# Performance work log

Hardware: AMD Instinct MI355X
Metric: run time of the kernel (lower is better)

The kernel has to match this reference:

```python
import jax, jax.numpy as jnp
import numpy as np

B, L, DM = 1, 512, 768
DS, DC, EX = 64, 4, 2
DI = EX * DM            # d_inner = 1536
DR = DM // 16           # dt_rank = 48


def setup_inputs() -> dict:
    key = jax.random.key(0)
    ks = jax.random.split(key, 12)
    s = 0.02
    inp = {
        "x": jax.random.normal(ks[0], (B, L, DM), dtype=jnp.float32),
        "ln_w": jnp.ones((DM,), jnp.float32),
        "ln_b": jnp.zeros((DM,), jnp.float32),
        "in_proj_w": jax.random.normal(ks[1], (2 * DI, DM), jnp.float32) * s,
        "conv_w": jax.random.normal(ks[2], (DI, 1, DC), jnp.float32) * s,
        "conv_b": jnp.zeros((DI,), jnp.float32),
        "x_proj_w": jax.random.normal(ks[3], (DR + 2 * DS, DI), jnp.float32) * s,
        "dt_proj_w": jax.random.normal(ks[4], (DI, DR), jnp.float32) * s,
        "dt_proj_b": jax.random.normal(ks[5], (DI,), jnp.float32) * s,
        "A_log": jnp.log(jnp.broadcast_to(jnp.arange(1, DS + 1, dtype=jnp.float32), (DI, DS))),
        "D": jnp.ones((DI,), jnp.float32),
        "out_proj_w": jax.random.normal(ks[6], (DM, DI), jnp.float32) * s,
    }
    return inp


def _layernorm(x, w, b, eps=1e-5):
    mu = jnp.mean(x, axis=-1, keepdims=True)
    var = jnp.mean((x - mu) ** 2, axis=-1, keepdims=True)
    return (x - mu) * jax.lax.rsqrt(var + eps) * w + b


def _causal_depthwise_conv(x, w, b):
    # x: [B, L, DI] -> conv over time, depthwise, causal (left pad DC-1)
    xc = jnp.transpose(x, (0, 2, 1))  # [B, DI, L]
    y = jax.lax.conv_general_dilated(
        xc, w, window_strides=(1,), padding=[(DC - 1, 0)],
        dimension_numbers=("NCH", "OIH", "NCH"), feature_group_count=DI)
    y = y + b[None, :, None]
    return jnp.transpose(y, (0, 2, 1))  # [B, L, DI]


def _selective_scan(deltaA, deltaB_u, C):
    # deltaA, deltaB_u: [B, L, DI, DS]; C: [B, L, DS]
    dA = jnp.transpose(deltaA, (1, 0, 2, 3))
    dBu = jnp.transpose(deltaB_u, (1, 0, 2, 3))
    Ct = jnp.transpose(C, (1, 0, 2))
    s0 = jnp.zeros(deltaA.shape[:1] + deltaA.shape[2:], deltaA.dtype).transpose(0, 1, 2)
    s0 = jnp.zeros((deltaA.shape[0], deltaA.shape[2], deltaA.shape[3]), deltaA.dtype)

    def step(s, inp):
        dA_t, dBu_t, C_t = inp
        s = dA_t * s + dBu_t                      # [B, DI, DS]
        y = jnp.einsum("bdn,bn->bd", s, C_t)      # [B, DI]
        return s, y

    _, ys = jax.lax.scan(step, s0, (dA, dBu, Ct))
    return jnp.transpose(ys, (1, 0, 2))           # [B, L, DI]


def reference(x, ln_w, ln_b, in_proj_w, conv_w, conv_b, x_proj_w,
              dt_proj_w, dt_proj_b, A_log, D, out_proj_w):
    residual = x
    h = _layernorm(x, ln_w, ln_b)
    xz = jnp.einsum("bld,ed->ble", h, in_proj_w)  # [B, L, 2*DI]
    x_in, z = jnp.split(xz, 2, axis=-1)
    x_in = jax.nn.silu(_causal_depthwise_conv(x_in, conv_w, conv_b))
    x_dbl = jnp.einsum("bld,ed->ble", x_in, x_proj_w)  # [B, L, DR+2*DS]
    dt, Bm, Cm = jnp.split(x_dbl, [DR, DR + DS], axis=-1)
    dt = jax.nn.softplus(jnp.einsum("blr,dr->bld", dt, dt_proj_w) + dt_proj_b)  # [B,L,DI]
    A = -jnp.exp(A_log)                                 # [DI, DS]
    deltaA = jnp.exp(dt[..., None] * A)                 # [B, L, DI, DS]
    deltaB_u = dt[..., None] * Bm[:, :, None, :] * x_in[..., None]
    y = _selective_scan(deltaA, deltaB_u, Cm)           # [B, L, DI]
    y = y + x_in * D
    y = y * jax.nn.silu(z)
    out = jnp.einsum("bld,ed->ble", y, out_proj_w)      # [B, L, DM]
    return residual + out
```

## Files before the change

kernel.cpp:

```cpp
#include <hip/hip_runtime.h>
#include <hip/hip_bf16.h>
#include <math.h>

#define L_SEQ 512
#define DM 768
#define DI 1536
#define DS 64
#define DC 4
#define DR 48
#define NBC 128
#define NP2 (NBC + DI)
#define NC 8
#define TC 64

typedef __attribute__((ext_vector_type(8))) short short8;
typedef __attribute__((ext_vector_type(4))) float float4v;

#define J_LN 512
#define J_WI (2 * DI * DM / 1024)
#define J_WBC (NBC * DI / 1024)
#define J_WO (DM * DI / 1024)
#define J_WEFF ((DI / 64) * (DI / 64))
#define PREP_GRID (J_LN + J_WI + J_WBC + J_WO + J_WEFF)

__device__ __forceinline__ float bp_add(float p, int addr) {
  return p + __int_as_float(__builtin_amdgcn_ds_bpermute(addr, __float_as_int(p)));
}
__device__ __forceinline__ float lane_read(float v, int t) {
  return __int_as_float(__builtin_amdgcn_readlane(__float_as_int(v), t));
}
__device__ __forceinline__ short f2bf(float v) {
  __hip_bfloat16 h = __float2bfloat16(v);
  return *reinterpret_cast<short*>(&h);
}
__device__ __forceinline__ short8 cvt8f(const float* p, bool valid) {
  float4 u = *(const float4*)(p);
  float4 v = *(const float4*)(p + 4);
  short8 r;
  r[0] = f2bf(u.x); r[1] = f2bf(u.y); r[2] = f2bf(u.z); r[3] = f2bf(u.w);
  r[4] = f2bf(v.x); r[5] = f2bf(v.y); r[6] = f2bf(v.z); r[7] = f2bf(v.w);
  if (!valid) r = (short8)0;
  return r;
}
__device__ __forceinline__ void cvt_blk(const float* __restrict__ s,
                                        short* __restrict__ d, int b) {
  int i = b * 1024 + threadIdx.x * 4;
  float4 v = *(const float4*)(s + i);
  short4 o; o.x = f2bf(v.x); o.y = f2bf(v.y); o.z = f2bf(v.z); o.w = f2bf(v.w);
  *(short4*)(d + i) = o;
}

__device__ __forceinline__ float4v gemm32_core(
    const short* __restrict__ A, int lda, const short* __restrict__ B, int ldb,
    int K, int bx, int by, int lane, int w, float4v* red) {
  int ks = K >> 2;
  int kbeg = w * ks;
  int fr = lane & 15, koff = (lane >> 4) * 8;
  int m0 = by * 32, n0 = bx * 32;
  const short* pA0 = A + (size_t)(m0 + fr) * lda + koff + kbeg;
  const short* pA1 = pA0 + (size_t)16 * lda;
  const short* pB0 = B + (size_t)(n0 + fr) * ldb + koff + kbeg;
  const short* pB1 = pB0 + (size_t)16 * ldb;
  float4v acc00 = (float4v){0.f,0.f,0.f,0.f}, acc01 = acc00;
  float4v acc10 = acc00, acc11 = acc00;
  short8 a0A = *(const short8*)(pA0);      short8 a1A = *(const short8*)(pA1);
  short8 b0A = *(const short8*)(pB0);      short8 b1A = *(const short8*)(pB1);
  short8 a0B = *(const short8*)(pA0 + 32); short8 a1B = *(const short8*)(pA1 + 32);
  short8 b0B = *(const short8*)(pB0 + 32); short8 b1B = *(const short8*)(pB1 + 32);
  for (int k0 = 0; k0 < ks; k0 += 64) {
    short8 ca0 = a0A, ca1 = a1A, cb0 = b0A, cb1 = b1A;
    short8 da0 = a0B, da1 = a1B, db0 = b0B, db1 = b1B;
    int nA = k0 + 64; if (nA >= ks) nA = 0;
    int nB = k0 + 96; if (nB >= ks) nB = 32;
    a0A = *(const short8*)(pA0 + nA); a1A = *(const short8*)(pA1 + nA);
    b0A = *(const short8*)(pB0 + nA); b1A = *(const short8*)(pB1 + nA);
    a0B = *(const short8*)(pA0 + nB); a1B = *(const short8*)(pA1 + nB);
    b0B = *(const short8*)(pB0 + nB); b1B = *(const short8*)(pB1 + nB);
    acc00 = __builtin_amdgcn_mfma_f32_16x16x32_bf16(ca0, cb0, acc00, 0, 0, 0);
    acc01 = __builtin_amdgcn_mfma_f32_16x16x32_bf16(ca0, cb1, acc01, 0, 0, 0);
    acc10 = __builtin_amdgcn_mfma_f32_16x16x32_bf16(ca1, cb0, acc10, 0, 0, 0);
    acc11 = __builtin_amdgcn_mfma_f32_16x16x32_bf16(ca1, cb1, acc11, 0, 0, 0);
    acc00 = __builtin_amdgcn_mfma_f32_16x16x32_bf16(da0, db0, acc00, 0, 0, 0);
    acc01 = __builtin_amdgcn_mfma_f32_16x16x32_bf16(da0, db1, acc01, 0, 0, 0);
    acc10 = __builtin_amdgcn_mfma_f32_16x16x32_bf16(da1, db0, acc10, 0, 0, 0);
    acc11 = __builtin_amdgcn_mfma_f32_16x16x32_bf16(da1, db1, acc11, 0, 0, 0);
  }
  red[(w * 4 + 0) * 64 + lane] = acc00;
  red[(w * 4 + 1) * 64 + lane] = acc01;
  red[(w * 4 + 2) * 64 + lane] = acc10;
  red[(w * 4 + 3) * 64 + lane] = acc11;
  __syncthreads();
  float4v v = red[(0 * 4 + w) * 64 + lane];
  v = v + red[(1 * 4 + w) * 64 + lane];
  v = v + red[(2 * 4 + w) * 64 + lane];
  v = v + red[(3 * 4 + w) * 64 + lane];
  return v;
}

__device__ __forceinline__ void trans_store32(float* t, float4v v,
                                              int lrow, int lcol, int tid,
                                              float* dst, size_t ldT, int m0) {
  __syncthreads();
#pragma unroll
  for (int r = 0; r < 4; ++r) t[lcol * 33 + lrow + r] = v[r];
  __syncthreads();
  int i = tid >> 3, j = (tid & 7) * 4;
  float4 o = make_float4(t[i * 33 + j], t[i * 33 + j + 1],
                         t[i * 33 + j + 2], t[i * 33 + j + 3]);
  *(float4*)&dst[(size_t)i * ldT + m0 + j] = o;
}

__global__ __launch_bounds__(256) void prep(
    const float* __restrict__ x, const float* __restrict__ lnw,
    const float* __restrict__ lnb, short* __restrict__ h,
    const float* __restrict__ wi, short* __restrict__ wib,
    const float* __restrict__ wx, const float* __restrict__ wdt,
    short* __restrict__ wcomb, const float* __restrict__ wo,
    short* __restrict__ wob) {
  __shared__ float ls[4], ls2[4];
  int b = blockIdx.x;
  int tid = threadIdx.x, lane = tid & 63, w = tid >> 6;
  if (b < J_LN) {
    int l = b;
    const float* xr = x + l * DM;
    float s = 0.f, s2 = 0.f;
    for (int i = tid; i < DM; i += 256) { float t = xr[i]; s += t; s2 += t * t; }
#pragma unroll
    for (int off = 32; off; off >>= 1) { s += __shfl_xor(s, off); s2 += __shfl_xor(s2, off); }
    if (lane == 0) { ls[w] = s; ls2[w] = s2; }
    __syncthreads();
    s = ls[0] + ls[1] + ls[2] + ls[3];
    s2 = ls2[0] + ls2[1] + ls2[2] + ls2[3];
    float mean = s * (1.f / DM);
    float var = s2 * (1.f / DM) - mean * mean;
    float rstd = rsqrtf(var + 1e-5f);
    for (int i = tid; i < DM; i += 256)
      h[l * DM + i] = f2bf((xr[i] - mean) * rstd * lnw[i] + lnb[i]);
    return;
  }
  b -= J_LN;
  if (b < J_WI) { cvt_blk(wi, wib, b); return; }
  b -= J_WI;
  if (b < J_WBC) { cvt_blk(wx + DR * DI, wcomb, b); return; }
  b -= J_WBC;
  if (b < J_WO) { cvt_blk(wo, wob, b); return; }
  b -= J_WO;
  {
    int tm = b / (DI / 64), tn = b % (DI / 64);
    int qi = w & 1, qj = w >> 1;
    int m0 = tm * 64 + qi * 32, n0 = tn * 64 + qj * 32;
    int fr = lane & 15, koff = (lane >> 4) * 8;
    const float* pA0 = wdt + (size_t)(m0 + fr) * DR;
    const float* pA1 = pA0 + (size_t)16 * DR;
    float4v a00 = (float4v){0.f,0.f,0.f,0.f}, a01 = a00, a10 = a00, a11 = a00;
#pragma unroll
    for (int k0 = 0; k0 < 64; k0 += 32) {
      bool valid = (k0 + koff) < DR;
      int off = valid ? k0 + koff : 0;
      short8 fa0 = cvt8f(pA0 + off, valid);
      short8 fa1 = cvt8f(pA1 + off, valid);
      short8 fb0, fb1;
#pragma unroll
      for (int j = 0; j < 8; ++j) {
        int r = k0 + koff + j;
        fb0[j] = valid ? f2bf(wx[(size_t)r * DI + n0 + fr]) : (short)0;
        fb1[j] = valid ? f2bf(wx[(size_t)r * DI + n0 + 16 + fr]) : (short)0;
      }
      a00 = __builtin_amdgcn_mfma_f32_16x16x32_bf16(fa0, fb0, a00, 0, 0, 0);
      a01 = __builtin_amdgcn_mfma_f32_16x16x32_bf16(fa0, fb1, a01, 0, 0, 0);
      a10 = __builtin_amdgcn_mfma_f32_16x16x32_bf16(fa1, fb0, a10, 0, 0, 0);
      a11 = __builtin_amdgcn_mfma_f32_16x16x32_bf16(fa1, fb1, a11, 0, 0, 0);
    }
    int rb = (lane >> 4) * 4, cb = lane & 15;
#pragma unroll
    for (int r = 0; r < 4; ++r) {
      wcomb[(size_t)(NBC + m0 + rb + r) * DI + n0 + cb]      = f2bf(a00[r]);
      wcomb[(size_t)(NBC + m0 + rb + r) * DI + n0 + 16 + cb] = f2bf(a01[r]);
      wcomb[(size_t)(NBC + m0 + 16 + rb + r) * DI + n0 + cb]      = f2bf(a10[r]);
      wcomb[(size_t)(NBC + m0 + 16 + rb + r) * DI + n0 + 16 + cb] = f2bf(a11[r]);
    }
  }
}

__global__ __launch_bounds__(256) void k_inproj(const short* __restrict__ h,
                                                const short* __restrict__ wi,
                                                float* __restrict__ xz_in,
                                                float* __restrict__ zt) {
  __shared__ float4v red[16 * 64];
  int tid = threadIdx.x, lane = tid & 63, w = tid >> 6;
  float4v v = gemm32_core(h, DM, wi, DM, DM, blockIdx.x, blockIdx.y, lane, w, red);
  int lrow = ((w & 1) << 4) + ((lane >> 4) << 2);
  int lcol = ((w >> 1) << 4) + (lane & 15);
  int m0 = blockIdx.y * 32, n0 = blockIdx.x * 32;
  if (n0 < DI) {
#pragma unroll
    for (int r = 0; r < 4; ++r)
      xz_in[(size_t)(m0 + lrow + r) * DI + n0 + lcol] = v[r];
  } else {
    trans_store32((float*)red, v, lrow, lcol, tid,
                  zt + (size_t)(n0 - DI) * L_SEQ, L_SEQ, m0);
  }
}

__global__ __launch_bounds__(256) void conv_silu_kernel(const float* __restrict__ xz_in,
                                                        const float* __restrict__ cw,
                                                        const float* __restrict__ cb,
                                                        short* __restrict__ xc_bf,
                                                        float* __restrict__ xct) {
  __shared__ float t2[64 * 34];
  int tid = threadIdx.x;
  int dloc = tid & 63, lseg = tid >> 6;
  int d0 = blockIdx.x * 64, l0 = blockIdx.y * 32;
  int d = d0 + dloc;
  int lb = l0 + lseg * 8;
  float xin[11];
#pragma unroll
  for (int i = 0; i < 11; ++i) {
    int l = lb - 3 + i;
    xin[i] = (l >= 0) ? xz_in[(size_t)l * DI + d] : 0.f;
  }
  float w0 = cw[d * 4 + 0], w1 = cw[d * 4 + 1];
  float w2 = cw[d * 4 + 2], w3 = cw[d * 4 + 3];
  float bias = cb[d];
#pragma unroll
  for (int j = 0; j < 8; ++j) {
    float acc = bias;
    acc = fmaf(w0, xin[j], acc);
    acc = fmaf(w1, xin[j + 1], acc);
    acc = fmaf(w2, xin[j + 2], acc);
    acc = fmaf(w3, xin[j + 3], acc);
    float sig = 1.f / (1.f + __expf(-acc));
    float v = acc * sig;
    xc_bf[(size_t)(lb + j) * DI + d] = f2bf(v);
    t2[dloc * 34 + lseg * 8 + j] = v;
  }
  __syncthreads();
  int row = tid >> 2, j4 = (tid & 3) * 8;
  const float* src = &t2[row * 34 + j4];
  float2 o0 = *(const float2*)(src + 0);
  float2 o1 = *(const float2*)(src + 2);
  float2 o2 = *(const float2*)(src + 4);
  float2 o3 = *(const float2*)(src + 6);
  float* dst = &xct[(size_t)(d0 + row) * L_SEQ + l0 + j4];
  *(float2*)(dst + 0) = o0; *(float2*)(dst + 2) = o1;
  *(float2*)(dst + 4) = o2; *(float2*)(dst + 6) = o3;
}

__global__ __launch_bounds__(256) void k_proj2(const short* __restrict__ xc,
                                               const short* __restrict__ wcomb,
                                               float* __restrict__ xdblBC,
                                               float* __restrict__ dtt,
                                               const float* __restrict__ bias) {
  __shared__ float4v red[16 * 64];
  int tid = threadIdx.x, lane = tid & 63, w = tid >> 6;
  float4v v = gemm32_core(xc, DI, wcomb, DI, DI, blockIdx.x, blockIdx.y,
                          lane, w, red);
  int lrow = ((w & 1) << 4) + ((lane >> 4) << 2);
  int lcol = ((w >> 1) << 4) + (lane & 15);
  int m0 = blockIdx.y * 32, n0 = blockIdx.x * 32;
  if (n0 < NBC) {
#pragma unroll
    for (int r = 0; r < 4; ++r)
      xdblBC[(size_t)(m0 + lrow + r) * NBC + n0 + lcol] = v[r];
  } else {
    float bi = bias[n0 - NBC + lcol];
#pragma unroll
    for (int r = 0; r < 4; ++r) {
      float t = v[r] + bi;
      v[r] = (t > 20.f) ? t : log1pf(__expf(t));
    }
    trans_store32((float*)red, v, lrow, lcol, tid,
                  dtt + (size_t)(n0 - NBC) * L_SEQ, L_SEQ, m0);
  }
}

__global__ __launch_bounds__(256) void scan_p1(const float* __restrict__ dtt,
                                               const float* __restrict__ xct,
                                               const float* __restrict__ xdblBC,
                                               const float* __restrict__ A_log,
                                               float* __restrict__ send,
                                               float* __restrict__ dts) {
  int lane = threadIdx.x & 63;
  int wid = threadIdx.x >> 6;
  int pair = blockIdx.x * 4 + wid;
  int c = __builtin_amdgcn_readfirstlane(pair / DI);
  int d = __builtin_amdgcn_readfirstlane(pair - (pair / DI) * DI);
  float A = -__expf(A_log[(size_t)d * DS + lane]);
  int l0 = c * TC;
  float dtv = dtt[(size_t)d * L_SEQ + l0 + lane];
  float xv  = xct[(size_t)d * L_SEQ + l0 + lane];
  const float* pB = xdblBC + (size_t)l0 * NBC + lane;
  float s = 0.f;
#pragma unroll 8
  for (int t = 0; t < TC; ++t) {
    float dt_c = lane_read(dtv, t);
    float x_c  = lane_read(xv, t);
    float B_c  = pB[(size_t)t * NBC];
    float dA = __expf(dt_c * A);
    s = fmaf(dA, s, dt_c * x_c * B_c);
  }
  float dsum = dtv;
  dsum = bp_add(dsum, (lane ^ 1) << 2);  dsum = bp_add(dsum, (lane ^ 2) << 2);
  dsum = bp_add(dsum, (lane ^ 4) << 2);  dsum = bp_add(dsum, (lane ^ 8) << 2);
  dsum = bp_add(dsum, (lane ^ 16) << 2); dsum = bp_add(dsum, (lane ^ 32) << 2);
  send[((size_t)c * DI + d) * DS + lane] = s;
  if (lane == 0) dts[c * DI + d] = dsum;
}

__global__ __launch_bounds__(256) void scan_p3(const float* __restrict__ dtt,
                                               const float* __restrict__ xct,
                                               const float* __restrict__ xdblBC,
                                               const float* __restrict__ A_log,
                                               const float* __restrict__ Dv,
                                               const float* __restrict__ zt,
                                               const float* __restrict__ send,
                                               const float* __restrict__ dts,
                                               short* __restrict__ y) {
  __shared__ float Pb[4][16][66];
  __shared__ float ys[64][5];
  int tid = threadIdx.x;
  int lane = tid & 63;
  int wid = tid >> 6;
  int pair = blockIdx.x * 4 + wid;
  int c = __builtin_amdgcn_readfirstlane(pair / DI);
  int d = __builtin_amdgcn_readfirstlane(pair - (pair / DI) * DI);
  float A = -__expf(A_log[(size_t)d * DS + lane]);
  float Dd = Dv[d];
  int l0 = c * TC;
  float dtv = dtt[(size_t)d * L_SEQ + l0 + lane];
  float xv  = xct[(size_t)d * L_SEQ + l0 + lane];
  float zv  = zt[(size_t)d * L_SEQ + l0 + lane];
  float s = 0.f;
  for (int cc = 0; cc < c; ++cc) {
    float P = __expf(A * dts[cc * DI + d]);
    s = fmaf(P, s, send[((size_t)cc * DI + d) * DS + lane]);
  }
  const float* pB = xdblBC + (size_t)l0 * NBC + lane;
  float yv = 0.f;
#pragma unroll
  for (int sb = 0; sb < 4; ++sb) {
    float P[16];
#pragma unroll
    for (int j = 0; j < 16; ++j) {
      int t = sb * 16 + j;
      float dt_c = lane_read(dtv, t);
      float x_c  = lane_read(xv, t);
      float B_c  = pB[(size_t)t * NBC];
      float C_c  = pB[(size_t)t * NBC + DS];
      float dA = __expf(dt_c * A);
      s = fmaf(dA, s, dt_c * x_c * B_c);
      P[j] = s * C_c;
    }
#pragma unroll
    for (int j = 0; j < 16; ++j) Pb[wid][j][lane] = P[j];
    int t4 = lane >> 2, q = lane & 3;
    const float* row = &Pb[wid][t4][q * 16];
    float part = 0.f;
#pragma unroll
    for (int k = 0; k < 8; ++k) {
      float2 v2 = *(const float2*)(row + 2 * k);
      part += v2.x + v2.y;
    }
    part = bp_add(part, (lane ^ 1) << 2);
    part = bp_add(part, (lane ^ 2) << 2);
    float got = __int_as_float(
        __builtin_amdgcn_ds_bpermute((lane & 15) << 4, __float_as_int(part)));
    yv = ((lane >> 4) == sb) ? got : yv;
  }
  float sig = 1.f / (1.f + __expf(-zv));
  ys[lane][wid] = (yv + xv * Dd) * (zv * sig);
  __syncthreads();
  if (tid < 64) {
    int d0 = (blockIdx.x * 4) % DI;
    short4 o;
    o.x = f2bf(ys[tid][0]); o.y = f2bf(ys[tid][1]);
    o.z = f2bf(ys[tid][2]); o.w = f2bf(ys[tid][3]);
    *(short4*)&y[(size_t)(l0 + tid) * DI + d0] = o;
  }
}

__global__ __launch_bounds__(256) void k_outproj(const short* __restrict__ y,
                                                 const short* __restrict__ wo,
                                                 const float* __restrict__ x,
                                                 float* __restrict__ out) {
  __shared__ float4v red[16 * 64];
  int tid = threadIdx.x, lane = tid & 63, w = tid >> 6;
  float4v v = gemm32_core(y, DI, wo, DI, DI, blockIdx.x, blockIdx.y, lane, w, red);
  int lrow = ((w & 1) << 4) + ((lane >> 4) << 2);
  int lcol = ((w >> 1) << 4) + (lane & 15);
  int row = blockIdx.y * 32 + lrow, col = blockIdx.x * 32 + lcol;
#pragma unroll
  for (int r = 0; r < 4; ++r)
    out[(size_t)(row + r) * DM + col] = v[r] + x[(size_t)(row + r) * DM + col];
}

extern "C" void kernel_launch(void* const* d_in, const int* in_sizes, int n_in,
                              void* d_out, int out_size, void* d_ws, size_t ws_size,
                              hipStream_t stream) {
  const float* x         = (const float*)d_in[0];
  const float* ln_w      = (const float*)d_in[1];
  const float* ln_b      = (const float*)d_in[2];
  const float* in_proj_w = (const float*)d_in[3];
  const float* conv_w    = (const float*)d_in[4];
  const float* conv_b    = (const float*)d_in[5];
  const float* x_proj_w  = (const float*)d_in[6];
  const float* dt_proj_w = (const float*)d_in[7];
  const float* dt_proj_b = (const float*)d_in[8];
  const float* A_log     = (const float*)d_in[9];
  const float* Dv        = (const float*)d_in[10];
  const float* out_proj_w= (const float*)d_in[11];
  float* out = (float*)d_out;

  float* ws = (float*)d_ws;
  float* xz_in  = ws;
  float* zt     = xz_in + 786432;
  float* xct    = zt + 786432;
  float* dtt    = xct + 786432;
  float* xdblBC = dtt + 786432;
  float* send   = xdblBC + 65536;
  float* dts    = send + 688128;
  float* fend   = dts + 10752;
  short* h_bf   = (short*)fend;
  short* wi_bf  = h_bf + 393216;
  short* wo_bf  = wi_bf + 2359296;
  short* wcomb  = wo_bf + 1179648;
  short* xc_bf  = wcomb + 2555904;
  short* y_bf   = xc_bf + 786432;

  prep<<<PREP_GRID, 256, 0, stream>>>(x, ln_w, ln_b, h_bf, in_proj_w, wi_bf,
                                      x_proj_w, dt_proj_w, wcomb,
                                      out_proj_w, wo_bf);

  k_inproj<<<dim3(2 * DI / 32, L_SEQ / 32), 256, 0, stream>>>(h_bf, wi_bf,
                                                              xz_in, zt);

  conv_silu_kernel<<<dim3(DI / 64, L_SEQ / 32), 256, 0, stream>>>(
      xz_in, conv_w, conv_b, xc_bf, xct);

  k_proj2<<<dim3(NP2 / 32, L_SEQ / 32), 256, 0, stream>>>(
      xc_bf, wcomb, xdblBC, dtt, dt_proj_b);

  scan_p1<<<((NC - 1) * DI) / 4, 256, 0, stream>>>(dtt, xct, xdblBC, A_log,
                                                   send, dts);
  scan_p3<<<(NC * DI) / 4, 256, 0, stream>>>(dtt, xct, xdblBC, A_log, Dv, zt,
                                             send, dts, y_bf);

  k_outproj<<<dim3(DM / 32, L_SEQ / 32), 256, 0, stream>>>(y_bf, wo_bf, x, out);
}
```

Before: 187.6 us.

## Fuse two-pass chunked scan into one block-level kernel with shared-memory carry

```diff
diff --git a/kernel.cpp b/kernel.cpp
--- a/kernel.cpp
+++ b/kernel.cpp
@@ -10,8 +10,8 @@
 #define DR 48
 #define NBC 128
 #define NP2 (NBC + DI)
-#define NC 8
-#define TC 64
+#define NCF 4
+#define TCF 128
 
 typedef __attribute__((ext_vector_type(8))) short short8;
 typedef __attribute__((ext_vector_type(4))) float float4v;
@@ -274,109 +274,113 @@
   }
 }
 
-__global__ __launch_bounds__(256) void scan_p1(const float* __restrict__ dtt,
-                                               const float* __restrict__ xct,
-                                               const float* __restrict__ xdblBC,
-                                               const float* __restrict__ A_log,
-                                               float* __restrict__ send,
-                                               float* __restrict__ dts) {
-  int lane = threadIdx.x & 63;
-  int wid = threadIdx.x >> 6;
-  int pair = blockIdx.x * 4 + wid;
-  int c = __builtin_amdgcn_readfirstlane(pair / DI);
-  int d = __builtin_amdgcn_readfirstlane(pair - (pair / DI) * DI);
-  float A = -__expf(A_log[(size_t)d * DS + lane]);
-  int l0 = c * TC;
-  float dtv = dtt[(size_t)d * L_SEQ + l0 + lane];
-  float xv  = xct[(size_t)d * L_SEQ + l0 + lane];
-  const float* pB = xdblBC + (size_t)l0 * NBC + lane;
-  float s = 0.f;
-#pragma unroll 8
-  for (int t = 0; t < TC; ++t) {
-    float dt_c = lane_read(dtv, t);
-    float x_c  = lane_read(xv, t);
-    float B_c  = pB[(size_t)t * NBC];
-    float dA = __expf(dt_c * A);
-    s = fmaf(dA, s, dt_c * x_c * B_c);
-  }
-  float dsum = dtv;
-  dsum = bp_add(dsum, (lane ^ 1) << 2);  dsum = bp_add(dsum, (lane ^ 2) << 2);
-  dsum = bp_add(dsum, (lane ^ 4) << 2);  dsum = bp_add(dsum, (lane ^ 8) << 2);
-  dsum = bp_add(dsum, (lane ^ 16) << 2); dsum = bp_add(dsum, (lane ^ 32) << 2);
-  send[((size_t)c * DI + d) * DS + lane] = s;
-  if (lane == 0) dts[c * DI + d] = dsum;
-}
-
-__global__ __launch_bounds__(256) void scan_p3(const float* __restrict__ dtt,
-                                               const float* __restrict__ xct,
-                                               const float* __restrict__ xdblBC,
-                                               const float* __restrict__ A_log,
-                                               const float* __restrict__ Dv,
-                                               const float* __restrict__ zt,
-                                               const float* __restrict__ send,
-                                               const float* __restrict__ dts,
-                                               short* __restrict__ y) {
-  __shared__ float Pb[4][16][66];
-  __shared__ float ys[64][5];
+__global__ __launch_bounds__(512) void scan_fused(const float* __restrict__ dtt,
+                                                  const float* __restrict__ xct,
+                                                  const float* __restrict__ xdblBC,
+                                                  const float* __restrict__ A_log,
+                                                  const float* __restrict__ Dv,
+                                                  const float* __restrict__ zt,
+                                                  short* __restrict__ y) {
+  __shared__ float Pb[8][16][66];
+  __shared__ float sendL[2][4][64];
+  __shared__ float dtsL[2][4];
+  __shared__ float ys[2][512];
   int tid = threadIdx.x;
   int lane = tid & 63;
-  int wid = tid >> 6;
-  int pair = blockIdx.x * 4 + wid;
-  int c = __builtin_amdgcn_readfirstlane(pair / DI);
-  int d = __builtin_amdgcn_readfirstlane(pair - (pair / DI) * DI);
+  int wv = tid >> 6;
+  int dloc = wv >> 2;
+  int c = wv & 3;
+  int d = blockIdx.x * 2 + dloc;
   float A = -__expf(A_log[(size_t)d * DS + lane]);
-  float Dd = Dv[d];
-  int l0 = c * TC;
-  float dtv = dtt[(size_t)d * L_SEQ + l0 + lane];
-  float xv  = xct[(size_t)d * L_SEQ + l0 + lane];
-  float zv  = zt[(size_t)d * L_SEQ + l0 + lane];
+  int l0 = c * TCF;
+  const float* dtp = dtt + (size_t)d * L_SEQ + l0;
+  const float* xp  = xct + (size_t)d * L_SEQ + l0;
+  const float* zp  = zt  + (size_t)d * L_SEQ + l0;
+  float dtv0 = dtp[lane], dtv1 = dtp[64 + lane];
+  float xv0  = xp[lane],  xv1  = xp[64 + lane];
+  float zv0  = zp[lane],  zv1  = zp[64 + lane];
+  const float* pB = xdblBC + (size_t)l0 * NBC + lane;
+
+  if (c < 3) {
+    float s = 0.f;
+#pragma unroll 8
+    for (int t = 0; t < 64; ++t) {
+      float dt_c = lane_read(dtv0, t);
+      float x_c  = lane_read(xv0, t);
+      float B_c  = pB[(size_t)t * NBC];
+      s = fmaf(__expf(dt_c * A), s, dt_c * x_c * B_c);
+    }
+#pragma unroll 8
+    for (int t = 0; t < 64; ++t) {
+      float dt_c = lane_read(dtv1, t);
+      float x_c  = lane_read(xv1, t);
+      float B_c  = pB[(size_t)(64 + t) * NBC];
+      s = fmaf(__expf(dt_c * A), s, dt_c * x_c * B_c);
+    }
+    float dsum = dtv0 + dtv1;
+    dsum = bp_add(dsum, (lane ^ 1) << 2);  dsum = bp_add(dsum, (lane ^ 2) << 2);
+    dsum = bp_add(dsum, (lane ^ 4) << 2);  dsum = bp_add(dsum, (lane ^ 8) << 2);
+    dsum = bp_add(dsum, (lane ^ 16) << 2); dsum = bp_add(dsum, (lane ^ 32) << 2);
+    sendL[dloc][c][lane] = s;
+    if (lane == 0) dtsL[dloc][c] = dsum;
+  }
+  __syncthreads();
+
   float s = 0.f;
   for (int cc = 0; cc < c; ++cc) {
-    float P = __expf(A * dts[cc * DI + d]);
-    s = fmaf(P, s, send[((size_t)cc * DI + d) * DS + lane]);
-  }
-  const float* pB = xdblBC + (size_t)l0 * NBC + lane;
-  float yv = 0.f;
-#pragma unroll
-  for (int sb = 0; sb < 4; ++sb) {
-    float P[16];
-#pragma unroll
-    for (int j = 0; j < 16; ++j) {
-      int t = sb * 16 + j;
-      float dt_c = lane_read(dtv, t);
-      float x_c  = lane_read(xv, t);
-      float B_c  = pB[(size_t)t * NBC];
-      float C_c  = pB[(size_t)t * NBC + DS];
-      float dA = __expf(dt_c * A);
-      s = fmaf(dA, s, dt_c * x_c * B_c);
-      P[j] = s * C_c;
-    }
-#pragma unroll
-    for (int j = 0; j < 16; ++j) Pb[wid][j][lane] = P[j];
-    int t4 = lane >> 2, q = lane & 3;
-    const float* row = &Pb[wid][t4][q * 16];
-    float part = 0.f;
-#pragma unroll
-    for (int k = 0; k < 8; ++k) {
-      float2 v2 = *(const float2*)(row + 2 * k);
-      part += v2.x + v2.y;
-    }
-    part = bp_add(part, (lane ^ 1) << 2);
-    part = bp_add(part, (lane ^ 2) << 2);
-    float got = __int_as_float(
-        __builtin_amdgcn_ds_bpermute((lane & 15) << 4, __float_as_int(part)));
-    yv = ((lane >> 4) == sb) ? got : yv;
-  }
-  float sig = 1.f / (1.f + __expf(-zv));
-  ys[lane][wid] = (yv + xv * Dd) * (zv * sig);
-  __syncthreads();
-  if (tid < 64) {
-    int d0 = (blockIdx.x * 4) % DI;
-    short4 o;
-    o.x = f2bf(ys[tid][0]); o.y = f2bf(ys[tid][1]);
-    o.z = f2bf(ys[tid][2]); o.w = f2bf(ys[tid][3]);
-    *(short4*)&y[(size_t)(l0 + tid) * DI + d0] = o;
-  }
+    float P = __expf(A * dtsL[dloc][cc]);
+    s = fmaf(P, s, sendL[dloc][cc][lane]);
+  }
+
+  float yout0 = 0.f, yout1 = 0.f;
+#pragma unroll
+  for (int half = 0; half < 2; ++half) {
+    float dtvh = half ? dtv1 : dtv0;
+    float xvh  = half ? xv1 : xv0;
+    float yv = 0.f;
+#pragma unroll
+    for (int sb = 0; sb < 4; ++sb) {
+      float P[16];
+#pragma unroll
+      for (int j = 0; j < 16; ++j) {
+        int t = sb * 16 + j;
+        float dt_c = lane_read(dtvh, t);
+        float x_c  = lane_read(xvh, t);
+        float B_c  = pB[(size_t)(half * 64 + t) * NBC];
+        float C_c  = pB[(size_t)(half * 64 + t) * NBC + DS];
+        s = fmaf(__expf(dt_c * A), s, dt_c * x_c * B_c);
+        P[j] = s * C_c;
+      }
+#pragma unroll
+      for (int j = 0; j < 16; ++j) Pb[wv][j][lane] = P[j];
+      int t4 = lane >> 2, q = lane & 3;
+      const float* row = &Pb[wv][t4][q * 16];
+      float part = 0.f;
+#pragma unroll
+      for (int k = 0; k < 8; ++k) {
+        float2 v2 = *(const float2*)(row + 2 * k);
+        part += v2.x + v2.y;
+      }
+      part = bp_add(part, (lane ^ 1) << 2);
+      part = bp_add(part, (lane ^ 2) << 2);
+      float got = __int_as_float(
+          __builtin_amdgcn_ds_bpermute((lane & 15) << 4, __float_as_int(part)));
+      yv = ((lane >> 4) == sb) ? got : yv;
+    }
+    if (half == 0) yout0 = yv; else yout1 = yv;
+  }
+
+  float Dd = Dv[d];
+  float sig0 = 1.f / (1.f + __expf(-zv0));
+  float sig1 = 1.f / (1.f + __expf(-zv1));
+  ys[dloc][l0 + lane]      = (yout0 + xv0 * Dd) * (zv0 * sig0);
+  ys[dloc][l0 + 64 + lane] = (yout1 + xv1 * Dd) * (zv1 * sig1);
+  __syncthreads();
+  int d0 = blockIdx.x * 2;
+  short2 o;
+  o.x = f2bf(ys[0][tid]);
+  o.y = f2bf(ys[1][tid]);
+  *(short2*)&y[(size_t)tid * DI + d0] = o;
 }
 
 __global__ __launch_bounds__(256) void k_outproj(const short* __restrict__ y,
@@ -417,9 +421,7 @@
   float* xct    = zt + 786432;
   float* dtt    = xct + 786432;
   float* xdblBC = dtt + 786432;
-  float* send   = xdblBC + 65536;
-  float* dts    = send + 688128;
-  float* fend   = dts + 10752;
+  float* fend   = xdblBC + 65536;
   short* h_bf   = (short*)fend;
   short* wi_bf  = h_bf + 393216;
   short* wo_bf  = wi_bf + 2359296;
@@ -440,10 +442,7 @@
   k_proj2<<<dim3(NP2 / 32, L_SEQ / 32), 256, 0, stream>>>(
       xc_bf, wcomb, xdblBC, dtt, dt_proj_b);
 
-  scan_p1<<<((NC - 1) * DI) / 4, 256, 0, stream>>>(dtt, xct, xdblBC, A_log,
-                                                   send, dts);
-  scan_p3<<<(NC * DI) / 4, 256, 0, stream>>>(dtt, xct, xdblBC, A_log, Dv, zt,
-                                             send, dts, y_bf);
+  scan_fused<<<DI / 2, 512, 0, stream>>>(dtt, xct, xdblBC, A_log, Dv, zt, y_bf);
 
   k_outproj<<<dim3(DM / 32, L_SEQ / 32), 256, 0, stream>>>(y_bf, wo_bf, x, out);
 }
```

After: 189.5 us. Within noise of the previous version (+1.0%).
